# Kernel tuning notes

Hardware: AMD Instinct MI355X
Metric: run time of the kernel (lower is better)

The kernel has to match this reference:

```python
import jax, jax.numpy as jnp
from jax import lax
import numpy as np

CHUNK = 1024  # query-chunk size; per-chunk intermediate is [B, CHUNK, M]


def _nn_min_sqdist(x, y):
    """For each point in x [B,N,D], squared distance to nearest point in y [B,M,D] -> [B,N].
    Computed in chunks over N so the full [B,N,M] matrix is never materialized."""
    B, N, D = x.shape
    y2 = jnp.sum(y * y, axis=-1)  # [B,M]
    n_chunks = N // CHUNK
    xs = x.reshape(B, n_chunks, CHUNK, D).transpose(1, 0, 2, 3)  # [n_chunks,B,CHUNK,D]

    def body(carry, xc):
        x2 = jnp.sum(xc * xc, axis=-1)  # [B,CHUNK]
        xy = jnp.einsum('bcd,bmd->bcm', xc, y)  # [B,CHUNK,M]
        d = x2[..., None] + y2[:, None, :] - 2.0 * xy
        return carry, jnp.min(d, axis=-1)  # [B,CHUNK]

    _, mins = lax.scan(body, None, xs)  # [n_chunks,B,CHUNK]
    return mins.transpose(1, 0, 2).reshape(B, N)


def setup_inputs() -> dict:
    key = jax.random.key(0)
    k1, k2 = jax.random.split(key)
    input1 = jax.random.normal(k1, (8, 16384, 3), dtype=jnp.float32)
    input2 = jax.random.normal(k2, (8, 16384, 3), dtype=jnp.float32)
    return {"input1": input1, "input2": input2}


def reference(input1, input2):
    # Chamfer nearest-neighbor squared distances, both directions.
    dist1 = _nn_min_sqdist(input1, input2)  # [B,N1]
    dist2 = _nn_min_sqdist(input2, input1)  # [B,N2]
    return (dist1, dist2)
```

## Files before the change

kernel.cpp:

```cpp
#include <hip/hip_runtime.h>


#define NB      8
#define NPTS    16384
#define THREADS 256
#define PPT     4
#define QPB     (THREADS * PPT)
#define TILE    2048
#define NSEG    4
#define YSEG    (NPTS / NSEG)

typedef float v2f __attribute__((ext_vector_type(2)));

__device__ __forceinline__ v2f pk_fma(v2f a, v2f b, v2f c) {
    v2f d;
    asm("v_pk_fma_f32 %0, %1, %2, %3" : "=v"(d) : "v"(a), "v"(b), "v"(c));
    return d;
}

__device__ __forceinline__ float min3f(float a, float b, float c) {
    float d;
    asm("v_min3_f32 %0, %1, %2, %3" : "=v"(d) : "v"(a), "v"(b), "v"(c));
    return d;
}

__global__ __launch_bounds__(THREADS, 4)
void nnd_kernel(const float* __restrict__ x1,
                const float* __restrict__ x2,
                float* __restrict__ out)
{
    constexpr int chunks = NPTS / QPB;
    const int bid   = blockIdx.x;
    const int yseg  = bid % NSEG;
    const int rem1  = bid / NSEG;
    const int chunk = rem1 % chunks;
    const int rem2  = rem1 / chunks;
    const int batch = rem2 % NB;
    const int dir   = rem2 / NB;

    const float* __restrict__ xq = (dir == 0) ? x1 : x2;
    const float* __restrict__ yr = (dir == 0) ? x2 : x1;
    const float* __restrict__ xb = xq + (size_t)batch * NPTS * 3;
    const float* __restrict__ yb = yr + (size_t)batch * NPTS * 3;
    float* __restrict__ ob = out + (size_t)dir * NB * NPTS
                                 + (size_t)batch * NPTS
                                 + (size_t)chunk * QPB;

    __shared__ __align__(16) float ysx[TILE];
    __shared__ __align__(16) float ysy[TILE];
    __shared__ __align__(16) float ysz[TILE];
    __shared__ __align__(16) float ysw[TILE];

    const int t = threadIdx.x;

    v2f nx[PPT], ny[PPT], nz[PPT];
    float sx[PPT];
    float a0[PPT], a1[PPT];
#pragma unroll
    for (int p = 0; p < PPT; ++p) {
        const int q = chunk * QPB + t + p * THREADS;
        const float qx = xb[3 * q + 0], qy = xb[3 * q + 1], qz = xb[3 * q + 2];
        sx[p] = qx * qx + qy * qy + qz * qz;
        const float mx = -2.0f * qx, my = -2.0f * qy, mz = -2.0f * qz;
        nx[p] = (v2f){mx, mx};
        ny[p] = (v2f){my, my};
        nz[p] = (v2f){mz, mz};
        a0[p] = INFINITY;
        a1[p] = INFINITY;
    }

    const int segbase = yseg * YSEG;

    for (int tile0 = 0; tile0 < YSEG; tile0 += TILE) {
        for (int k = t; k < TILE; k += THREADS) {
            const float* yp = yb + 3 * (size_t)(segbase + tile0 + k);
            const float a = yp[0], b = yp[1], c = yp[2];
            ysx[k] = a; ysy[k] = b; ysz[k] = c;
            ysw[k] = a * a + b * b + c * c;
        }
        __syncthreads();

#pragma unroll 2
        for (int j = 0; j < TILE; j += 4) {
            const v2f x01 = *(const v2f*)&ysx[j];
            const v2f x23 = *(const v2f*)&ysx[j + 2];
            const v2f y01 = *(const v2f*)&ysy[j];
            const v2f y23 = *(const v2f*)&ysy[j + 2];
            const v2f z01 = *(const v2f*)&ysz[j];
            const v2f z23 = *(const v2f*)&ysz[j + 2];
            const v2f w01 = *(const v2f*)&ysw[j];
            const v2f w23 = *(const v2f*)&ysw[j + 2];

#pragma unroll
            for (int p = 0; p < PPT; ++p) {
                v2f t01 = pk_fma(nz[p], z01, w01);
                t01 = pk_fma(ny[p], y01, t01);
                t01 = pk_fma(nx[p], x01, t01);
                v2f t23 = pk_fma(nz[p], z23, w23);
                t23 = pk_fma(ny[p], y23, t23);
                t23 = pk_fma(nx[p], x23, t23);
                a0[p] = min3f(t01.x, t01.y, a0[p]);
                a1[p] = min3f(t23.x, t23.y, a1[p]);
            }
        }
        __syncthreads();
    }

#pragma unroll
    for (int p = 0; p < PPT; ++p) {
        float d = sx[p] + fminf(a0[p], a1[p]);
        d = fmaxf(d, 0.0f);
        atomicMin((unsigned int*)&ob[t + p * THREADS], __float_as_uint(d));
    }
}

extern "C" void kernel_launch(void* const* d_in, const int* in_sizes, int n_in,
                              void* d_out, int out_size, void* d_ws, size_t ws_size,
                              hipStream_t stream) {
    const float* x1 = (const float*)d_in[0];
    const float* x2 = (const float*)d_in[1];
    float* out = (float*)d_out;

    hipMemsetAsync(out, 0xFF, (size_t)out_size * sizeof(float), stream);

    constexpr int total_blocks = 2 * NB * (NPTS / QPB) * NSEG;
    nnd_kernel<<<dim3(total_blocks), dim3(THREADS), 0, stream>>>(x1, x2, out);
}
```

Baseline: 359.9 us.

## Use float4 LDS tiles, more queries per thread, and a workspace min-reduction

Raises queries per thread from 4 to 8 and splits the reference set into 8 segments. Reference points are stored in LDS as one float4 per point (x, y, z and squared norm) instead of four separate arrays. The packed v_pk_fma_f32 path is replaced by scalar FMAs. When the workspace is large enough, each segment writes partial minima to the workspace and a separate kernel reduces them, replacing the memset plus atomicMin. This trades twice as many scalar FMA instructions and an extra launch for fewer atomics and wider LDS loads. The non-atomic path also drops the clamp to zero, so outputs can come out slightly negative.

```diff
diff --git a/kernel.cpp b/kernel.cpp
--- a/kernel.cpp
+++ b/kernel.cpp
@@ -4,19 +4,13 @@
 #define NB      8
 #define NPTS    16384
 #define THREADS 256
-#define PPT     4
+#define PPT     8
 #define QPB     (THREADS * PPT)
-#define TILE    2048
-#define NSEG    4
+#define CHUNKS  (NPTS / QPB)
+#define NSEG    8
 #define YSEG    (NPTS / NSEG)
-
-typedef float v2f __attribute__((ext_vector_type(2)));
-
-__device__ __forceinline__ v2f pk_fma(v2f a, v2f b, v2f c) {
-    v2f d;
-    asm("v_pk_fma_f32 %0, %1, %2, %3" : "=v"(d) : "v"(a), "v"(b), "v"(c));
-    return d;
-}
+#define TILE    1024
+#define TOTQ    (2 * NB * NPTS)
 
 __device__ __forceinline__ float min3f(float a, float b, float c) {
     float d;
@@ -24,83 +18,62 @@
     return d;
 }
 
+template<int ATOMIC>
 __global__ __launch_bounds__(THREADS, 4)
-void nnd_kernel(const float* __restrict__ x1,
-                const float* __restrict__ x2,
-                float* __restrict__ out)
+void nnd_main(const float* __restrict__ x1, const float* __restrict__ x2,
+              float* __restrict__ dst)
 {
-    constexpr int chunks = NPTS / QPB;
     const int bid   = blockIdx.x;
-    const int yseg  = bid % NSEG;
-    const int rem1  = bid / NSEG;
-    const int chunk = rem1 % chunks;
-    const int rem2  = rem1 / chunks;
-    const int batch = rem2 % NB;
-    const int dir   = rem2 / NB;
+    const int seg   = bid & (NSEG - 1);
+    const int rem1  = bid >> 3;
+    const int chunk = rem1 & (CHUNKS - 1);
+    const int rem2  = rem1 >> 3;
+    const int batch = rem2 & (NB - 1);
+    const int dir   = rem2 >> 3;
 
-    const float* __restrict__ xq = (dir == 0) ? x1 : x2;
-    const float* __restrict__ yr = (dir == 0) ? x2 : x1;
-    const float* __restrict__ xb = xq + (size_t)batch * NPTS * 3;
-    const float* __restrict__ yb = yr + (size_t)batch * NPTS * 3;
-    float* __restrict__ ob = out + (size_t)dir * NB * NPTS
-                                 + (size_t)batch * NPTS
-                                 + (size_t)chunk * QPB;
+    const float* __restrict__ xb = (dir ? x2 : x1) + (size_t)batch * NPTS * 3;
+    const float* __restrict__ yb = (dir ? x1 : x2) + (size_t)batch * NPTS * 3;
 
-    __shared__ __align__(16) float ysx[TILE];
-    __shared__ __align__(16) float ysy[TILE];
-    __shared__ __align__(16) float ysz[TILE];
-    __shared__ __align__(16) float ysw[TILE];
+    float* __restrict__ po = dst
+        + (ATOMIC ? (size_t)0 : (size_t)seg * TOTQ)
+        + (size_t)dir * NB * NPTS + (size_t)batch * NPTS + (size_t)chunk * QPB;
+
+    __shared__ float4 yt[TILE];
 
     const int t = threadIdx.x;
 
-    v2f nx[PPT], ny[PPT], nz[PPT];
-    float sx[PPT];
-    float a0[PPT], a1[PPT];
+    float nx[PPT], ny[PPT], nz[PPT], sx[PPT], ac[PPT];
 #pragma unroll
     for (int p = 0; p < PPT; ++p) {
         const int q = chunk * QPB + t + p * THREADS;
-        const float qx = xb[3 * q + 0], qy = xb[3 * q + 1], qz = xb[3 * q + 2];
-        sx[p] = qx * qx + qy * qy + qz * qz;
-        const float mx = -2.0f * qx, my = -2.0f * qy, mz = -2.0f * qz;
-        nx[p] = (v2f){mx, mx};
-        ny[p] = (v2f){my, my};
-        nz[p] = (v2f){mz, mz};
-        a0[p] = INFINITY;
-        a1[p] = INFINITY;
+        const float X = xb[3 * q + 0], Y = xb[3 * q + 1], Z = xb[3 * q + 2];
+        sx[p] = fmaf(X, X, fmaf(Y, Y, Z * Z));
+        nx[p] = -2.0f * X;
+        ny[p] = -2.0f * Y;
+        nz[p] = -2.0f * Z;
+        ac[p] = INFINITY;
     }
 
-    const int segbase = yseg * YSEG;
-
-    for (int tile0 = 0; tile0 < YSEG; tile0 += TILE) {
-        for (int k = t; k < TILE; k += THREADS) {
-            const float* yp = yb + 3 * (size_t)(segbase + tile0 + k);
+    const int ybeg = seg * YSEG;
+    for (int tb = ybeg; tb < ybeg + YSEG; tb += TILE) {
+#pragma unroll
+        for (int s = 0; s < TILE / THREADS; ++s) {
+            const int k = t + s * THREADS;
+            const float* yp = yb + 3 * (size_t)(tb + k);
             const float a = yp[0], b = yp[1], c = yp[2];
-            ysx[k] = a; ysy[k] = b; ysz[k] = c;
-            ysw[k] = a * a + b * b + c * c;
+            yt[k] = make_float4(a, b, c, fmaf(a, a, fmaf(b, b, c * c)));
         }
         __syncthreads();
 
 #pragma unroll 2
-        for (int j = 0; j < TILE; j += 4) {
-            const v2f x01 = *(const v2f*)&ysx[j];
-            const v2f x23 = *(const v2f*)&ysx[j + 2];
-            const v2f y01 = *(const v2f*)&ysy[j];
-            const v2f y23 = *(const v2f*)&ysy[j + 2];
-            const v2f z01 = *(const v2f*)&ysz[j];
-            const v2f z23 = *(const v2f*)&ysz[j + 2];
-            const v2f w01 = *(const v2f*)&ysw[j];
-            const v2f w23 = *(const v2f*)&ysw[j + 2];
-
+        for (int j = 0; j < TILE; j += 2) {
+            const float4 p0 = yt[j];
+            const float4 p1 = yt[j + 1];
 #pragma unroll
             for (int p = 0; p < PPT; ++p) {
-                v2f t01 = pk_fma(nz[p], z01, w01);
-                t01 = pk_fma(ny[p], y01, t01);
-                t01 = pk_fma(nx[p], x01, t01);
-                v2f t23 = pk_fma(nz[p], z23, w23);
-                t23 = pk_fma(ny[p], y23, t23);
-                t23 = pk_fma(nx[p], x23, t23);
-                a0[p] = min3f(t01.x, t01.y, a0[p]);
-                a1[p] = min3f(t23.x, t23.y, a1[p]);
+                const float d0 = fmaf(nx[p], p0.x, fmaf(ny[p], p0.y, fmaf(nz[p], p0.z, p0.w)));
+                const float d1 = fmaf(nx[p], p1.x, fmaf(ny[p], p1.y, fmaf(nz[p], p1.z, p1.w)));
+                ac[p] = min3f(d0, d1, ac[p]);
             }
         }
         __syncthreads();
@@ -108,10 +81,25 @@
 
 #pragma unroll
     for (int p = 0; p < PPT; ++p) {
-        float d = sx[p] + fminf(a0[p], a1[p]);
-        d = fmaxf(d, 0.0f);
-        atomicMin((unsigned int*)&ob[t + p * THREADS], __float_as_uint(d));
+        const float v = sx[p] + ac[p];
+        if (ATOMIC) {
+            const float vc = fmaxf(v, 0.0f);
+            atomicMin((unsigned int*)&po[t + p * THREADS], __float_as_uint(vc));
+        } else {
+            po[t + p * THREADS] = v;
+        }
     }
+}
+
+__global__ __launch_bounds__(THREADS)
+void nnd_reduce(const float* __restrict__ part, float* __restrict__ out)
+{
+    const int i = blockIdx.x * THREADS + threadIdx.x;
+    float m = part[i];
+#pragma unroll
+    for (int s = 1; s < NSEG; ++s)
+        m = fminf(m, part[(size_t)s * TOTQ + i]);
+    out[i] = m;
 }
 
 extern "C" void kernel_launch(void* const* d_in, const int* in_sizes, int n_in,
@@ -121,8 +109,15 @@
     const float* x2 = (const float*)d_in[1];
     float* out = (float*)d_out;
 
-    hipMemsetAsync(out, 0xFF, (size_t)out_size * sizeof(float), stream);
+    constexpr int grid = 2 * NB * CHUNKS * NSEG;
+    const size_t part_bytes = (size_t)NSEG * TOTQ * 4;
 
-    constexpr int total_blocks = 2 * NB * (NPTS / QPB) * NSEG;
-    nnd_kernel<<<dim3(total_blocks), dim3(THREADS), 0, stream>>>(x1, x2, out);
+    if (ws_size >= part_bytes) {
+        float* part = (float*)d_ws;
+        nnd_main<0><<<dim3(grid), dim3(THREADS), 0, stream>>>(x1, x2, part);
+        nnd_reduce<<<dim3(TOTQ / THREADS), dim3(THREADS), 0, stream>>>(part, out);
+    } else {
+        hipMemsetAsync(out, 0xFF, (size_t)out_size * sizeof(float), stream);
+        nnd_main<1><<<dim3(grid), dim3(THREADS), 0, stream>>>(x1, x2, out);
+    }
 }
```

Result: slower. 376.5 us (+4.6%).
